# Kernel tuning notes

Measured on AMD Instinct MI355X. Metric: run time of the kernel, lower is better.

The kernel has to match this reference:

```python
import jax, jax.numpy as jnp
import numpy as np
from jax.scipy.special import xlogy

D_MODEL = 768
NUM_HEADS = 12
DEPTH = D_MODEL // NUM_HEADS
FEAT = D_MODEL // 6  # embedding_size // 6
LN2 = 0.6931471805599453


def positional_encodings(L):
    # pos: [1, 2L-1] from -(L-1) .. (L-1)
    pos = jnp.arange(-L + 1, L, dtype=jnp.float32)[None]
    apos = jnp.abs(pos)                      # [1, 2L-1]
    sgn = jnp.sign(pos)[..., None]           # [1, 2L-1, 1]
    Lf = jnp.float32(L)
    # f_exponential
    max_range = jnp.log(Lf) / LN2
    half_life = 2.0 ** jnp.linspace(3.0, max_range, FEAT)  # [F]
    exp1 = jnp.exp(-LN2 / half_life * apos[..., None])     # [1,2L-1,F]
    # f_central_mask
    cw = 2.0 ** jnp.arange(1, FEAT + 1, dtype=jnp.float32) - 1.0
    cm1 = (cw > apos[..., None]).astype(jnp.float32)
    # f_gamma
    stdv = Lf / (2.0 * FEAT)
    mean = jnp.linspace(Lf / FEAT, Lf, FEAT)
    conc = (mean / stdv) ** 2
    rate = mean / stdv ** 2
    x = apos[..., None]
    logp = xlogy(conc - 1.0, x) - rate * x - (jax.lax.lgamma(conc) - conc * jnp.log(rate))
    probs = jnp.exp(logp)
    gam1 = probs / jnp.max(probs)
    return jnp.concatenate([exp1, exp1 * sgn, cm1, cm1 * sgn, gam1, gam1 * sgn], axis=-1)  # [1,2L-1,d_model]


def relative_shift(x):
    # x: [B, H, L, 2L-1] -> [B, H, L, L] (Transformer-XL shift trick)
    B, H, t1, t2m1 = x.shape
    t2 = t2m1 + 1
    x = jnp.concatenate([jnp.zeros_like(x[..., :1]), x], axis=-1)  # [B,H,t1,t2]
    x = x.reshape(B, H, t2, t1)[:, :, 1:, :].reshape(B, H, t1, t2 - 1)
    return x[..., : (t2 + 1) // 2]


def split_heads(x):
    B, L, _ = x.shape
    return x.reshape(B, L, NUM_HEADS, DEPTH).transpose(0, 2, 1, 3)  # [B,H,L,D]


def setup_inputs() -> dict:
    key = jax.random.key(0)
    ks = jax.random.split(key, 12)
    B, L = 1, 2048
    s = 0.03
    return {
        "v": jax.random.normal(ks[0], (B, L, D_MODEL), jnp.float32),
        "k": jax.random.normal(ks[1], (B, L, D_MODEL), jnp.float32),
        "q": jax.random.normal(ks[2], (B, L, D_MODEL), jnp.float32),
        "mask": jax.random.randint(ks[3], (B, 1, 1, L), 0, 2, jnp.int32),
        "Wq": jax.random.normal(ks[4], (D_MODEL, D_MODEL), jnp.float32) * s,
        "Wk": jax.random.normal(ks[5], (D_MODEL, D_MODEL), jnp.float32) * s,
        "Wv": jax.random.normal(ks[6], (D_MODEL, D_MODEL), jnp.float32) * s,
        "Wrk": jax.random.normal(ks[7], (D_MODEL, D_MODEL), jnp.float32) * s,
        "r_w": jax.random.normal(ks[8], (1, NUM_HEADS, 1, DEPTH), jnp.float32) * 0.5,
        "r_r": jax.random.normal(ks[9], (1, NUM_HEADS, 1, DEPTH), jnp.float32) * 0.5,
        "Wo": jax.random.normal(ks[10], (D_MODEL, D_MODEL), jnp.float32) * s,
        "bo": jnp.zeros((D_MODEL,), jnp.float32),
    }


def reference(v, k, q, mask, Wq, Wk, Wv, Wrk, r_w, r_r, Wo, bo):
    B, L, _ = q.shape
    qh = split_heads(q @ Wq) / jnp.sqrt(jnp.float32(DEPTH))  # [B,H,L,D]
    kh = split_heads(k @ Wk)
    vh = split_heads(v @ Wv)
    pe = positional_encodings(L)                              # [1,2L-1,d_model]
    r_k = (pe @ Wrk).reshape(1, 2 * L - 1, NUM_HEADS, DEPTH).transpose(0, 2, 1, 3)[0]  # [H,2L-1,D]
    content_logits = jnp.einsum('bhqd,bhkd->bhqk', qh + r_w, kh)
    relative_logits = jnp.einsum('bhqd,hrd->bhqr', qh + r_r, r_k)  # [B,H,L,2L-1]
    logits = content_logits + relative_shift(relative_logits)     # [B,H,L,L]
    logits = jnp.where(mask == 1, -10000.0, logits)
    attention_map = jax.nn.softmax(logits, axis=-1)
    attended = jnp.einsum('bhqk,bhkd->bhqd', attention_map, vh)
    concat = attended.transpose(0, 2, 1, 3).reshape(B, L, D_MODEL)
    output = concat @ Wo + bo
    return output, attention_map
```

## Files before the change

### kernel.cpp

```cpp
#include <hip/hip_runtime.h>
#include <hip/hip_bf16.h>
#include <math.h>

typedef unsigned short u16;
typedef __bf16 bf16x8_t __attribute__((ext_vector_type(8)));
typedef u16 u16x8 __attribute__((ext_vector_type(8)));
typedef u16 u16x4 __attribute__((ext_vector_type(4)));
typedef float f32x4 __attribute__((ext_vector_type(4)));

#define NH 12
#define LQ 2048
#define DM 768
#define DH 64
#define NR 4095
#define LN2F 0.6931471805599453f

__device__ __forceinline__ u16 f2bf(float f){
  unsigned x = __float_as_uint(f);
  return (u16)((x + 0x7fffu + ((x >> 16) & 1u)) >> 16);
}
__device__ __forceinline__ float bf2f(u16 u){ return __uint_as_float(((unsigned)u) << 16); }

__device__ __forceinline__ f32x4 MFMA(u16x8 a, u16x8 b, f32x4 c){
  return __builtin_amdgcn_mfma_f32_16x16x32_bf16(
      __builtin_bit_cast(bf16x8_t, a), __builtin_bit_cast(bf16x8_t, b), c, 0, 0, 0);
}

__launch_bounds__(256)
__global__ void prep_kernel(const float* q, const float* k, const float* v,
                            const float* W0, const float* W1, const float* W2,
                            const float* W3, const float* W4,
                            u16* qb, u16* kb, u16* vb,
                            u16* T0, u16* T1, u16* T2, u16* T3, u16* T4,
                            double* __restrict__ logx, double* __restrict__ Cf){
  __shared__ u16 tile[64 * 72];
  const int bid = blockIdx.x;
  const int t = threadIdx.x;
  if (bid < 2304){
    int z = bid / 768, b = bid - z * 768;
    const float* src = (z == 0) ? q : (z == 1) ? k : v;
    u16* dst = (z == 0) ? qb : (z == 1) ? kb : vb;
    int base = (b * 256 + t) * 8;
    f32x4 a0 = *(const f32x4*)(src + base);
    f32x4 a1 = *(const f32x4*)(src + base + 4);
    u16x8 o;
    #pragma unroll
    for (int j = 0; j < 4; j++){ o[j] = f2bf(a0[j]); o[4 + j] = f2bf(a1[j]); }
    *(u16x8*)(dst + base) = o;
  } else if (bid < 3024){
    int r = bid - 2304;
    int z = r / 144, rem = r - z * 144;
    int k0 = (rem % 12) * 64, n0 = (rem / 12) * 64;
    const float* W = (z == 0) ? W0 : (z == 1) ? W1 : (z == 2) ? W2 : (z == 3) ? W3 : W4;
    u16* T = (z == 0) ? T0 : (z == 1) ? T1 : (z == 2) ? T2 : (z == 3) ? T3 : T4;
    {
      int kr = t >> 2, ng = (t & 3) * 16;
      const float* p = W + (size_t)(k0 + kr) * DM + n0 + ng;
      u16x8 o0, o1;
      #pragma unroll
      for (int j = 0; j < 8; j++){ o0[j] = f2bf(p[j]); o1[j] = f2bf(p[8 + j]); }
      *(u16x8*)&tile[kr * 72 + ng] = o0;
      *(u16x8*)&tile[kr * 72 + ng + 8] = o1;
    }
    __syncthreads();
    {
      int nr = t >> 2, kg = (t & 3) * 16;
      u16x8 o0, o1;
      #pragma unroll
      for (int j = 0; j < 8; j++){
        o0[j] = tile[(kg + j) * 72 + nr];
        o1[j] = tile[(kg + j + 8) * 72 + nr];
      }
      u16* qp = T + (size_t)(n0 + nr) * DM + k0 + kg;
      *(u16x8*)qp = o0;
      *(u16x8*)(qp + 8) = o1;
    }
  } else {
    int i = (bid - 3024) * 256 + t;
    if (i < 2048) logx[i] = (i > 0) ? log((double)i) : 0.0;
    if (i < 128){
      double fp1 = (double)(i + 1);
      double conc = 4.0 * fp1 * fp1;
      double rate = 0.25 * fp1;
      Cf[i] = conc * log(rate) - lgamma(conc);
    }
  }
}

__global__ void gamma_probs_kernel(const double* __restrict__ logx,
                                   const double* __restrict__ Cf,
                                   float* __restrict__ gamtab,
                                   unsigned* __restrict__ gmax){
  int idx = blockIdx.x * 256 + threadIdx.x;
  int x = idx >> 7, f = idx & 127;
  double fp1 = (double)(f + 1);
  double conc = 4.0 * fp1 * fp1;
  double rate = 0.25 * fp1;
  double xl = (x > 0) ? (conc - 1.0) * logx[x] : 0.0;
  double logp = xl - rate * (double)x + Cf[f];
  float p = __expf((float)logp);
  gamtab[idx] = p;
  float m = p;
  #pragma unroll
  for (int off = 1; off < 64; off <<= 1) m = fmaxf(m, __shfl_xor(m, off));
  if ((threadIdx.x & 63) == 0) atomicMax(gmax, __float_as_uint(m));
}

__global__ void pe_kernel(const float* __restrict__ gamtab,
                          const unsigned* __restrict__ gmax,
                          u16* __restrict__ peb){
  int idx = blockIdx.x * 256 + threadIdx.x;
  if (idx >= NR * DM) return;
  int p = idx / DM;
  int c = idx - p * DM;
  int f = c & 127;
  int kind = c >> 7;
  int pos = p - (LQ - 1);
  int apos = pos < 0 ? -pos : pos;
  float sgn = (pos > 0) ? 1.f : ((pos < 0) ? -1.f : 0.f);
  float v;
  int grp = kind >> 1;
  if (grp == 0){
    float hl = exp2f(3.f + 8.f * (float)f / 127.f);
    v = expf(-(LN2F / hl) * (float)apos);
  } else if (grp == 1){
    float cw = exp2f((float)(f + 1)) - 1.f;
    v = (cw > (float)apos) ? 1.f : 0.f;
  } else {
    float gm = __uint_as_float(*gmax);
    v = gamtab[apos * 128 + f] / gm;
  }
  if (kind & 1) v *= sgn;
  peb[idx] = f2bf(v);
}

#define ASTR 72
__launch_bounds__(256)
__global__ void proj128_kernel(const u16* __restrict__ qb, const u16* __restrict__ kb,
                               const u16* __restrict__ vb, const u16* __restrict__ peb,
                               const u16* __restrict__ WqT, const u16* __restrict__ WkT,
                               const u16* __restrict__ WvT, const u16* __restrict__ WrkT,
                               u16* __restrict__ qh, u16* __restrict__ kh,
                               u16* __restrict__ vt, u16* __restrict__ rk){
  __shared__ u16 At[128 * ASTR];
  __shared__ u16 Wt[128 * ASTR];
  const int bid = blockIdx.x;
  int z, bx, by;
  if (bid < 288){ z = bid / 96; int t = bid - z * 96; bx = t & 15; by = t >> 4; }
  else          { z = 3; int t = bid - 288; bx = t & 31; by = t >> 5; }
  const u16* A  = (z == 0) ? qb : (z == 1) ? kb : (z == 2) ? vb : peb;
  const u16* WT = (z == 0) ? WqT : (z == 1) ? WkT : (z == 2) ? WvT : WrkT;
  const int m0 = bx * 128, n0 = by * 128;
  const int tid = threadIdx.x;
  const int w = tid >> 6, l = tid & 63, lr = l & 15, lg = l >> 4;
  const int moff = (w & 1) * 64, noff = (w >> 1) * 64;
  f32x4 acc[4][4] = {};
  const int srow = tid >> 1, sg = (tid & 1) * 32;
  for (int k0 = 0; k0 < DM; k0 += 64){
    {
      int m = m0 + srow;
      u16x8 a0 = {}, a1 = {}, a2 = {}, a3 = {};
      if (z < 3 || m < NR){
        const u16* ap = A + (size_t)m * DM + k0 + sg;
        a0 = *(const u16x8*)ap;
        a1 = *(const u16x8*)(ap + 8);
        a2 = *(const u16x8*)(ap + 16);
        a3 = *(const u16x8*)(ap + 24);
      }
      u16* sp = &At[srow * ASTR + sg];
      *(u16x8*)sp = a0;
      *(u16x8*)(sp + 8) = a1;
      *(u16x8*)(sp + 16) = a2;
      *(u16x8*)(sp + 24) = a3;
      const u16* wp = WT + (size_t)(n0 + srow) * DM + k0 + sg;
      u16* wq = &Wt[srow * ASTR + sg];
      *(u16x8*)wq = *(const u16x8*)wp;
      *(u16x8*)(wq + 8) = *(const u16x8*)(wp + 8);
      *(u16x8*)(wq + 16) = *(const u16x8*)(wp + 16);
      *(u16x8*)(wq + 24) = *(const u16x8*)(wp + 24);
    }
    __syncthreads();
    #pragma unroll
    for (int kc = 0; kc < 2; kc++){
      u16x8 af[4], bf[4];
      #pragma unroll
      for (int mi = 0; mi < 4; mi++)
        af[mi] = *(u16x8*)&At[(moff + mi * 16 + lr) * ASTR + kc * 32 + lg * 8];
      #pragma unroll
      for (int ni = 0; ni < 4; ni++)
        bf[ni] = *(u16x8*)&Wt[(noff + ni * 16 + lr) * ASTR + kc * 32 + lg * 8];
      #pragma unroll
      for (int mi = 0; mi < 4; mi++)
        #pragma unroll
        for (int ni = 0; ni < 4; ni++)
          acc[mi][ni] = MFMA(af[mi], bf[ni], acc[mi][ni]);
    }
    __syncthreads();
  }
  if (z == 2){
    #pragma unroll
    for (int mi = 0; mi < 4; mi++)
      #pragma unroll
      for (int ni = 0; ni < 4; ni++){
        int m = m0 + moff + mi * 16 + lg * 4;
        int n = n0 + noff + ni * 16 + lr;
        u16x4 ov;
        #pragma unroll
        for (int j = 0; j < 4; j++) ov[j] = f2bf(acc[mi][ni][j]);
        *(u16x4*)(vt + ((size_t)(n >> 6) * DH + (n & 63)) * LQ + m) = ov;
      }
  } else if (z == 3){
    #pragma unroll
    for (int mi = 0; mi < 4; mi++)
      #pragma unroll
      for (int ni = 0; ni < 4; ni++)
        #pragma unroll
        for (int j = 0; j < 4; j++){
          int m = m0 + moff + mi * 16 + lg * 4 + j;
          int n = n0 + noff + ni * 16 + lr;
          if (m < NR)
            rk[((size_t)(n >> 6) * NR + m) * DH + (n & 63)] = f2bf(acc[mi][ni][j]);
        }
  } else {
    u16* outb = (z == 0) ? qh : kh;
    const float scale = (z == 0) ? 0.125f : 1.f;
    #pragma unroll
    for (int mi = 0; mi < 4; mi++)
      #pragma unroll
      for (int ni = 0; ni < 4; ni++)
        #pragma unroll
        for (int j = 0; j < 4; j++){
          int m = m0 + moff + mi * 16 + lg * 4 + j;
          int n = n0 + noff + ni * 16 + lr;
          outb[((size_t)(n >> 6) * LQ + m) * DH + (n & 63)] = f2bf(acc[mi][ni][j] * scale);
        }
  }
}

#define GSTRB 72
__launch_bounds__(256)
__global__ void gemm_out_kernel(const u16* __restrict__ A, const u16* __restrict__ WT,
                                float* __restrict__ outf, const float* __restrict__ bias){
  __shared__ u16 At[64 * GSTRB];
  __shared__ u16 Wt[64 * GSTRB];
  const int m0 = blockIdx.x * 64, n0 = blockIdx.y * 64;
  const int tid = threadIdx.x;
  const int w = tid >> 6, l = tid & 63, lr = l & 15, lg = l >> 4;
  const int moff = (w & 1) * 32, noff = (w >> 1) * 32;
  f32x4 acc[2][2] = {};
  const int arow = tid >> 2, akg = (tid & 3) * 16;
  for (int k0 = 0; k0 < DM; k0 += 64){
    {
      const u16* ap = A + (size_t)(m0 + arow) * DM + k0 + akg;
      *(u16x8*)&At[arow * GSTRB + akg] = *(const u16x8*)ap;
      *(u16x8*)&At[arow * GSTRB + akg + 8] = *(const u16x8*)(ap + 8);
      const u16* wp = WT + (size_t)(n0 + arow) * DM + k0 + akg;
      *(u16x8*)&Wt[arow * GSTRB + akg] = *(const u16x8*)wp;
      *(u16x8*)&Wt[arow * GSTRB + akg + 8] = *(const u16x8*)(wp + 8);
    }
    __syncthreads();
    #pragma unroll
    for (int kc = 0; kc < 2; kc++){
      u16x8 af0 = *(u16x8*)&At[(moff + lr) * GSTRB + kc * 32 + lg * 8];
      u16x8 af1 = *(u16x8*)&At[(moff + 16 + lr) * GSTRB + kc * 32 + lg * 8];
      u16x8 bf0 = *(u16x8*)&Wt[(noff + lr) * GSTRB + kc * 32 + lg * 8];
      u16x8 bf1 = *(u16x8*)&Wt[(noff + 16 + lr) * GSTRB + kc * 32 + lg * 8];
      acc[0][0] = MFMA(af0, bf0, acc[0][0]);
      acc[0][1] = MFMA(af0, bf1, acc[0][1]);
      acc[1][0] = MFMA(af1, bf0, acc[1][0]);
      acc[1][1] = MFMA(af1, bf1, acc[1][1]);
    }
    __syncthreads();
  }
  #pragma unroll
  for (int mi = 0; mi < 2; mi++)
    #pragma unroll
    for (int ni = 0; ni < 2; ni++)
      #pragma unroll
      for (int j = 0; j < 4; j++){
        int m = m0 + moff + mi * 16 + lg * 4 + j;
        int n = n0 + noff + ni * 16 + lr;
        __builtin_nontemporal_store(acc[mi][ni][j] + bias[n], &outf[(size_t)m * DM + n]);
      }
}

#define QB 16
#define DSTR 16
#define DROWS 288
#define PSTR 264
#define SLABU (DROWS * DSTR)
#define SMEM_ATTN (8 * SLABU * 2 + 1024)
__launch_bounds__(512, 4)
__global__ void attn_kernel(const u16* __restrict__ qh, const u16* __restrict__ kh,
                            const u16* __restrict__ vt, const u16* __restrict__ rk,
                            const int* __restrict__ mask,
                            const float* __restrict__ r_w, const float* __restrict__ r_r,
                            float* __restrict__ map, u16* __restrict__ att){
  extern __shared__ char smem[];
  u16* RP = (u16*)smem;
  float* redm = (float*)(smem + 8 * SLABU * 2);
  float* redl = redm + 128;
  const int bid = blockIdx.x;
  const int swz = (bid & 7) * 192 + (bid >> 3);
  const int h = swz >> 7, q0 = (swz & 127) * QB;
  const int tid = threadIdx.x, w = tid >> 6, l = tid & 63, lr = l & 15, lg = l >> 4;
  const int roff = (LQ - 1) - q0 - (QB - 1);
  const int kb = w * 256;
  u16* slab = RP + w * SLABU;

  u16x8 a1[2], a2[2];
  #pragma unroll
  for (int kc = 0; kc < 2; kc++){
    u16x8 qv = *(const u16x8*)(qh + (size_t)(h * LQ + q0 + lr) * DH + kc * 32 + lg * 8);
    #pragma unroll
    for (int j = 0; j < 8; j++){
      int d = kc * 32 + lg * 8 + j;
      float f = bf2f(qv[j]);
      a1[kc][j] = f2bf(f + r_w[h * DH + d]);
      a2[kc][j] = f2bf(f + r_r[h * DH + d]);
    }
  }

  unsigned mbits = 0;
  {
    #pragma unroll
    for (int i = 0; i < 4; i++){
      int nt = lg + 4 * i;
      int mv = mask[kb + nt * 16 + lr];
      mbits |= ((unsigned)(mv & 1)) << nt;
    }
    mbits |= __shfl_xor(mbits, 16);
    mbits |= __shfl_xor(mbits, 32);
  }

  __builtin_amdgcn_s_setprio(1);
  #pragma unroll 4
  for (int t = 0; t < 17; t++){
    int r = roff + kb + t * 16 + lr;
    if (r > NR - 1) r = NR - 1;
    const u16* rp = rk + (size_t)(h * NR + r) * DH + lg * 8;
    u16x8 b0 = *(const u16x8*)(rp);
    u16x8 b1 = *(const u16x8*)(rp + 32);
    f32x4 racc = {};
    racc = MFMA(a2[0], b0, racc);
    racc = MFMA(a2[1], b1, racc);
    int lc = t * 16 + lr;
    #pragma unroll
    for (int j = 0; j < 4; j++){
      int ql = lg * 4 + j;
      slab[(lc + ql) * DSTR + ql] = f2bf(racc[j]);
    }
  }
  __asm__ volatile("s_waitcnt lgkmcnt(0)" ::: "memory");
  __builtin_amdgcn_sched_barrier(0);

  f32x4 s[16];
  #pragma unroll
  for (int nt = 0; nt < 16; nt++){
    const u16* kp = kh + (size_t)(h * LQ + kb + nt * 16 + lr) * DH + lg * 8;
    u16x8 b0 = *(const u16x8*)(kp);
    u16x8 b1 = *(const u16x8*)(kp + 32);
    f32x4 sv = {};
    sv = MFMA(a1[0], b0, sv);
    sv = MFMA(a1[1], b1, sv);
    int mv = (mbits >> nt) & 1;
    u16x4 g = *(u16x4*)&slab[(nt * 16 + lr + (QB - 1)) * DSTR + lg * 4];
    #pragma unroll
    for (int j = 0; j < 4; j++){
      float x = sv[j] + bf2f(g[j]);
      sv[j] = mv ? -10000.f : x;
    }
    s[nt] = sv;
  }
  __builtin_amdgcn_s_setprio(0);

  float fm[4];
  #pragma unroll
  for (int j = 0; j < 4; j++){
    float mx = -3.0e38f;
    #pragma unroll
    for (int nt = 0; nt < 16; nt++) mx = fmaxf(mx, s[nt][j]);
    #pragma unroll
    for (int off = 1; off < 16; off <<= 1) mx = fmaxf(mx, __shfl_xor(mx, off));
    if (lr == 0) redm[w * QB + lg * 4 + j] = mx;
  }
  __syncthreads();
  #pragma unroll
  for (int j = 0; j < 4; j++){
    int ql = lg * 4 + j;
    float mx = redm[ql];
    #pragma unroll
    for (int w2 = 1; w2 < 8; w2++) mx = fmaxf(mx, redm[w2 * QB + ql]);
    fm[j] = mx;
  }

  float ls[4] = {0.f, 0.f, 0.f, 0.f};
  #pragma unroll
  for (int nt = 0; nt < 16; nt++)
    #pragma unroll
    for (int j = 0; j < 4; j++){
      float p = __expf(s[nt][j] - fm[j]);
      ls[j] += p;
      slab[(lg * 4 + j) * PSTR + nt * 16 + lr] = f2bf(p);
    }
  #pragma unroll
  for (int j = 0; j < 4; j++){
    float sum = ls[j];
    #pragma unroll
    for (int off = 1; off < 16; off <<= 1) sum += __shfl_xor(sum, off);
    if (lr == 0) redl[w * QB + lg * 4 + j] = sum;
  }
  __syncthreads();
  float inv[4];
  #pragma unroll
  for (int j = 0; j < 4; j++){
    int ql = lg * 4 + j;
    float d = redl[ql];
    #pragma unroll
    for (int w2 = 1; w2 < 8; w2++) d += redl[w2 * QB + ql];
    inv[j] = 1.f / d;
  }

  {
    int qrow = tid >> 5, cb = (tid & 31) * 8;
    float dsum = redl[qrow];
    #pragma unroll
    for (int w2 = 1; w2 < 8; w2++) dsum += redl[w2 * QB + qrow];
    float invr = 1.f / dsum;
    float* mrow = map + (size_t)(h * LQ + q0 + qrow) * LQ;
    #pragma unroll
    for (int it = 0; it < 8; it++){
      u16x8 pv = *(u16x8*)&RP[it * SLABU + qrow * PSTR + cb];
      f32x4 o0, o1;
      #pragma unroll
      for (int j = 0; j < 4; j++){
        o0[j] = bf2f(pv[j]) * invr;
        o1[j] = bf2f(pv[4 + j]) * invr;
      }
      int c = cb + it * 256;
      __builtin_nontemporal_store(o0, (f32x4*)(mrow + c));
      __builtin_nontemporal_store(o1, (f32x4*)(mrow + c + 4));
    }
  }

  __builtin_amdgcn_s_setprio(1);
  f32x4 o[4] = {};
  #pragma unroll
  for (int kc2 = 0; kc2 < 8; kc2++){
    u16x8 pa = *(u16x8*)&slab[lr * PSTR + kc2 * 32 + lg * 8];
    #pragma unroll
    for (int ni = 0; ni < 4; ni++){
      u16x8 vv = *(const u16x8*)(vt + (size_t)(h * DH + ni * 16 + lr) * LQ + kb + kc2 * 32 + lg * 8);
      o[ni] = MFMA(pa, vv, o[ni]);
    }
  }
  __builtin_amdgcn_s_setprio(0);
  __syncthreads();

  float* Op = (float*)smem;
  #pragma unroll
  for (int ni = 0; ni < 4; ni++)
    #pragma unroll
    for (int j = 0; j < 4; j++)
      Op[(w * QB + lg * 4 + j) * 64 + ni * 16 + lr] = o[ni][j] * inv[j];
  __syncthreads();
  {
    int q = tid >> 5, dg = (tid & 31) * 2;
    float acc0 = 0.f, acc1 = 0.f;
    #pragma unroll
    for (int w2 = 0; w2 < 8; w2++){
      acc0 += Op[(w2 * QB + q) * 64 + dg];
      acc1 += Op[(w2 * QB + q) * 64 + dg + 1];
    }
    unsigned pk = (unsigned)f2bf(acc0) | ((unsigned)f2bf(acc1) << 16);
    *(unsigned*)(att + (size_t)(q0 + q) * DM + h * DH + dg) = pk;
  }
}

extern "C" void kernel_launch(void* const* d_in, const int* in_sizes, int n_in,
                              void* d_out, int out_size, void* d_ws, size_t ws_size,
                              hipStream_t stream){
  const float* v_in = (const float*)d_in[0];
  const float* k_in = (const float*)d_in[1];
  const float* q_in = (const float*)d_in[2];
  const int*   mask = (const int*)d_in[3];
  const float* Wq   = (const float*)d_in[4];
  const float* Wk   = (const float*)d_in[5];
  const float* Wv   = (const float*)d_in[6];
  const float* Wrk  = (const float*)d_in[7];
  const float* r_w  = (const float*)d_in[8];
  const float* r_r  = (const float*)d_in[9];
  const float* Wo   = (const float*)d_in[10];
  const float* bo   = (const float*)d_in[11];

  char* ws = (char*)d_ws;
  u16* qh  = (u16*)(ws + 0);
  u16* kh  = (u16*)(ws + 3145728);
  u16* vt  = (u16*)(ws + 6291456);
  u16* rk  = (u16*)(ws + 9437184);
  u16* qb  = (u16*)(ws + 15728640);
  u16* kb  = (u16*)(ws + 18874368);
  u16* vb  = (u16*)(ws + 22020096);
  u16* WqT = (u16*)(ws + 25165824);
  u16* WkT = (u16*)(ws + 26345472);
  u16* WvT = (u16*)(ws + 27525120);
  u16* WrkT= (u16*)(ws + 28704768);
  u16* WoT = (u16*)(ws + 29884416);
  u16* peb = (u16*)(ws + 31064064);
  u16* att = (u16*)(ws + 37355520);
  float* gamtab = (float*)(ws + 43646976);
  unsigned* gmax = (unsigned*)(ws + 44695552);
  double* logx = (double*)(ws + 44695616);
  double* Cf   = (double*)(ws + 44712000);

  float* out0 = (float*)d_out;
  float* map  = out0 + (size_t)LQ * DM;

  hipMemsetAsync(gmax, 0, 4, stream);
  prep_kernel<<<dim3(3032), 256, 0, stream>>>(q_in, k_in, v_in,
                                              Wq, Wk, Wv, Wrk, Wo,
                                              qb, kb, vb,
                                              WqT, WkT, WvT, WrkT, WoT,
                                              logx, Cf);
  gamma_probs_kernel<<<1024, 256, 0, stream>>>(logx, Cf, gamtab, gmax);
  pe_kernel<<<(NR * DM + 255) / 256, 256, 0, stream>>>(gamtab, gmax, peb);

  proj128_kernel<<<dim3(480), 256, 0, stream>>>(qb, kb, vb, peb,
                                                WqT, WkT, WvT, WrkT,
                                                qh, kh, vt, rk);

  hipFuncSetAttribute((const void*)attn_kernel,
                      hipFuncAttributeMaxDynamicSharedMemorySize, SMEM_ATTN);
  attn_kernel<<<dim3((LQ / QB) * NH), 512, SMEM_ATTN, stream>>>(qh, kh, vt, rk, mask,
                                                                r_w, r_r, map, att);
  gemm_out_kernel<<<dim3(32, 12), 256, 0, stream>>>(att, WoT, out0, bo);
}
```

Baseline: 267.2 us.

## Store projected Q/K/V/Rk in MFMA-fragment-native layout for contiguous attention loads

The projection kernel now writes qh, kh, vt and rk in a pre-swizzled layout that matches the 16x16x32 MFMA operand fragment order. Each lane's 8-element operand then sits contiguously with its neighbours, so the attention kernel's global loads become fully coalesced 1KB-per-wave reads instead of strided row gathers. The rk tensor is padded to 4096 rows and its last row is duplicated, which removes the clamp on r. The cost is scattered 2-byte stores in the projection epilogue, including for V, which previously used 8-byte vector stores.

```diff
diff --git a/kernel.cpp b/kernel.cpp
--- a/kernel.cpp
+++ b/kernel.cpp
@@ -140,8 +140,8 @@
                                const u16* __restrict__ vb, const u16* __restrict__ peb,
                                const u16* __restrict__ WqT, const u16* __restrict__ WkT,
                                const u16* __restrict__ WvT, const u16* __restrict__ WrkT,
-                               u16* __restrict__ qh, u16* __restrict__ kh,
-                               u16* __restrict__ vt, u16* __restrict__ rk){
+                               u16* __restrict__ qhF, u16* __restrict__ khF,
+                               u16* __restrict__ vtF, u16* __restrict__ rkF){
   __shared__ u16 At[128 * ASTR];
   __shared__ u16 Wt[128 * ASTR];
   const int bid = blockIdx.x;
@@ -197,44 +197,42 @@
     }
     __syncthreads();
   }
-  if (z == 2){
-    #pragma unroll
-    for (int mi = 0; mi < 4; mi++)
-      #pragma unroll
-      for (int ni = 0; ni < 4; ni++){
-        int m = m0 + moff + mi * 16 + lg * 4;
+  #pragma unroll
+  for (int mi = 0; mi < 4; mi++)
+    #pragma unroll
+    for (int ni = 0; ni < 4; ni++)
+      #pragma unroll
+      for (int j = 0; j < 4; j++){
+        int m = m0 + moff + mi * 16 + lg * 4 + j;
         int n = n0 + noff + ni * 16 + lr;
-        u16x4 ov;
-        #pragma unroll
-        for (int j = 0; j < 4; j++) ov[j] = f2bf(acc[mi][ni][j]);
-        *(u16x4*)(vt + ((size_t)(n >> 6) * DH + (n & 63)) * LQ + m) = ov;
+        int hh = n >> 6, d = n & 63;
+        float val = acc[mi][ni][j];
+        if (z == 0){
+          size_t idx = ((((size_t)hh * 128 + (m >> 4)) * 2 + (d >> 5)) * 64
+                        + ((d >> 3) & 3) * 16 + (m & 15)) * 8 + (d & 7);
+          qhF[idx] = f2bf(val * 0.125f);
+        } else if (z == 1){
+          size_t idx = ((((size_t)hh * 128 + (m >> 4)) * 2 + (d >> 5)) * 64
+                        + ((d >> 3) & 3) * 16 + (m & 15)) * 8 + (d & 7);
+          khF[idx] = f2bf(val);
+        } else if (z == 2){
+          size_t idx = ((((size_t)hh * 4 + (d >> 4)) * 64 + (m >> 5)) * 64
+                        + ((m >> 3) & 3) * 16 + (d & 15)) * 8 + (m & 7);
+          vtF[idx] = f2bf(val);
+        } else {
+          if (m < NR){
+            u16 bv = f2bf(val);
+            size_t idx = ((((size_t)hh * 256 + (m >> 4)) * 2 + (d >> 5)) * 64
+                          + ((d >> 3) & 3) * 16 + (m & 15)) * 8 + (d & 7);
+            rkF[idx] = bv;
+            if (m == NR - 1){
+              size_t idx2 = ((((size_t)hh * 256 + 255) * 2 + (d >> 5)) * 64
+                             + ((d >> 3) & 3) * 16 + 15) * 8 + (d & 7);
+              rkF[idx2] = bv;
+            }
+          }
+        }
       }
-  } else if (z == 3){
-    #pragma unroll
-    for (int mi = 0; mi < 4; mi++)
-      #pragma unroll
-      for (int ni = 0; ni < 4; ni++)
-        #pragma unroll
-        for (int j = 0; j < 4; j++){
-          int m = m0 + moff + mi * 16 + lg * 4 + j;
-          int n = n0 + noff + ni * 16 + lr;
-          if (m < NR)
-            rk[((size_t)(n >> 6) * NR + m) * DH + (n & 63)] = f2bf(acc[mi][ni][j]);
-        }
-  } else {
-    u16* outb = (z == 0) ? qh : kh;
-    const float scale = (z == 0) ? 0.125f : 1.f;
-    #pragma unroll
-    for (int mi = 0; mi < 4; mi++)
-      #pragma unroll
-      for (int ni = 0; ni < 4; ni++)
-        #pragma unroll
-        for (int j = 0; j < 4; j++){
-          int m = m0 + moff + mi * 16 + lg * 4 + j;
-          int n = n0 + noff + ni * 16 + lr;
-          outb[((size_t)(n >> 6) * LQ + m) * DH + (n & 63)] = f2bf(acc[mi][ni][j] * scale);
-        }
-  }
 }
 
 #define GSTRB 72
@@ -291,8 +289,8 @@
 #define SLABU (DROWS * DSTR)
 #define SMEM_ATTN (8 * SLABU * 2 + 1024)
 __launch_bounds__(512, 4)
-__global__ void attn_kernel(const u16* __restrict__ qh, const u16* __restrict__ kh,
-                            const u16* __restrict__ vt, const u16* __restrict__ rk,
+__global__ void attn_kernel(const u16* __restrict__ qhF, const u16* __restrict__ khF,
+                            const u16* __restrict__ vtF, const u16* __restrict__ rkF,
                             const int* __restrict__ mask,
                             const float* __restrict__ r_w, const float* __restrict__ r_r,
                             float* __restrict__ map, u16* __restrict__ att){
@@ -306,12 +304,14 @@
   const int tid = threadIdx.x, w = tid >> 6, l = tid & 63, lr = l & 15, lg = l >> 4;
   const int roff = (LQ - 1) - q0 - (QB - 1);
   const int kb = w * 256;
+  const int kt0 = kb >> 4;
+  const int rt0 = (roff + kb) >> 4;
   u16* slab = RP + w * SLABU;
 
   u16x8 a1[2], a2[2];
   #pragma unroll
   for (int kc = 0; kc < 2; kc++){
-    u16x8 qv = *(const u16x8*)(qh + (size_t)(h * LQ + q0 + lr) * DH + kc * 32 + lg * 8);
+    u16x8 qv = *(const u16x8*)(qhF + ((((size_t)h * 128 + (q0 >> 4)) * 2 + kc) * 64 + l) * 8);
     #pragma unroll
     for (int j = 0; j < 8; j++){
       int d = kc * 32 + lg * 8 + j;
@@ -336,11 +336,9 @@
   __builtin_amdgcn_s_setprio(1);
   #pragma unroll 4
   for (int t = 0; t < 17; t++){
-    int r = roff + kb + t * 16 + lr;
-    if (r > NR - 1) r = NR - 1;
-    const u16* rp = rk + (size_t)(h * NR + r) * DH + lg * 8;
+    const u16* rp = rkF + (((size_t)h * 256 + rt0 + t) * 2) * 512 + l * 8;
     u16x8 b0 = *(const u16x8*)(rp);
-    u16x8 b1 = *(const u16x8*)(rp + 32);
+    u16x8 b1 = *(const u16x8*)(rp + 512);
     f32x4 racc = {};
     racc = MFMA(a2[0], b0, racc);
     racc = MFMA(a2[1], b1, racc);
@@ -357,9 +355,9 @@
   f32x4 s[16];
   #pragma unroll
   for (int nt = 0; nt < 16; nt++){
-    const u16* kp = kh + (size_t)(h * LQ + kb + nt * 16 + lr) * DH + lg * 8;
+    const u16* kp = khF + (((size_t)h * 128 + kt0 + nt) * 2) * 512 + l * 8;
     u16x8 b0 = *(const u16x8*)(kp);
-    u16x8 b1 = *(const u16x8*)(kp + 32);
+    u16x8 b1 = *(const u16x8*)(kp + 512);
     f32x4 sv = {};
     sv = MFMA(a1[0], b0, sv);
     sv = MFMA(a1[1], b1, sv);
@@ -450,8 +448,8 @@
     u16x8 pa = *(u16x8*)&slab[lr * PSTR + kc2 * 32 + lg * 8];
     #pragma unroll
     for (int ni = 0; ni < 4; ni++){
-      u16x8 vv = *(const u16x8*)(vt + (size_t)(h * DH + ni * 16 + lr) * LQ + kb + kc2 * 32 + lg * 8);
-      o[ni] = MFMA(pa, vv, o[ni]);
+      const u16* vp = vtF + ((((size_t)h * 4 + ni) * 64 + (kb >> 5) + kc2) * 64 + l) * 8;
+      o[ni] = MFMA(pa, *(const u16x8*)vp, o[ni]);
     }
   }
   __builtin_amdgcn_s_setprio(0);
@@ -494,10 +492,10 @@
   const float* bo   = (const float*)d_in[11];
 
   char* ws = (char*)d_ws;
-  u16* qh  = (u16*)(ws + 0);
-  u16* kh  = (u16*)(ws + 3145728);
-  u16* vt  = (u16*)(ws + 6291456);
-  u16* rk  = (u16*)(ws + 9437184);
+  u16* qhF = (u16*)(ws + 0);
+  u16* khF = (u16*)(ws + 3145728);
+  u16* vtF = (u16*)(ws + 6291456);
+  u16* rkF = (u16*)(ws + 9437184);
   u16* qb  = (u16*)(ws + 15728640);
   u16* kb  = (u16*)(ws + 18874368);
   u16* vb  = (u16*)(ws + 22020096);
@@ -527,11 +525,11 @@
 
   proj128_kernel<<<dim3(480), 256, 0, stream>>>(qb, kb, vb, peb,
                                                 WqT, WkT, WvT, WrkT,
-                                                qh, kh, vt, rk);
+                                                qhF, khF, vtF, rkF);
 
   hipFuncSetAttribute((const void*)attn_kernel,
                       hipFuncAttributeMaxDynamicSharedMemorySize, SMEM_ATTN);
-  attn_kernel<<<dim3((LQ / QB) * NH), 512, SMEM_ATTN, stream>>>(qh, kh, vt, rk, mask,
+  attn_kernel<<<dim3((LQ / QB) * NH), 512, SMEM_ATTN, stream>>>(qhF, khF, vtF, rkF, mask,
                                                                 r_w, r_r, map, att);
   gemm_out_kernel<<<dim3(32, 12), 256, 0, stream>>>(att, WoT, out0, bo);
 }
```

Measured after the change: 216.8 us. -18.9%, faster.
